# Kernel optimization log

Measured on AMD Instinct MI355X. Metric: run time of the kernel, lower is better.

Reference implementation:

```python
import jax, jax.numpy as jnp
import numpy as np

# dims
IMG = 24; B = 2; C = 3; N = IMG * IMG + 1        # 577 tokens (patch size 1 + cls)
DIM = 512; DEPTH = 2; H = 8; DH = 64; MLP = 2048; NCLS = 1000
SW = 32      # sliding window size
CB = 16      # compress block size
CS = 4       # compress block sliding stride
SB = 64      # selection block size
KSEL = 4     # num selected blocks


def _ln(x, g, b):
    m = x.mean(-1, keepdims=True)
    v = ((x - m) ** 2).mean(-1, keepdims=True)
    return (x - m) * jax.lax.rsqrt(v + 1e-5) * g + b


# gather rows per (batch, head): t [n, d], i [n, m] -> [n, m, d]
_gather = jax.vmap(jax.vmap(lambda t, i: t[i]))


def _sparse_attn(x, Wq, Wk, Wv, Wg, Wo, kpe, vpe, Wkc, Wvc):
    """Native-sparse-attention (non-causal): compress + top-k block select + sliding window,
    combined with per-head sigmoid gates computed from the input."""
    b, n, _ = x.shape
    split = lambda t: t.reshape(b, n, H, DH).transpose(0, 2, 1, 3)   # [b,h,n,dh]
    q = split(x @ Wq); k = split(x @ Wk); v = split(x @ Wv)
    scale = DH ** -0.5

    # ---- compressed branch: overlapping blocks of size CB, stride CS, MLP-compressed ----
    nc = -(-n // CS)
    pad = (nc - 1) * CS + CB - n
    kp = jnp.pad(k, ((0, 0), (0, 0), (0, pad), (0, 0)))
    vp = jnp.pad(v, ((0, 0), (0, 0), (0, pad), (0, 0)))
    widx = jnp.arange(nc)[:, None] * CS + jnp.arange(CB)[None, :]    # [nc, CB]
    kw = kp[:, :, widx] + kpe                                        # [b,h,nc,CB,dh]
    vw = vp[:, :, widx] + vpe
    ck = kw.reshape(b, H, nc, CB * DH) @ Wkc                         # [b,h,nc,dh]
    cv = vw.reshape(b, H, nc, CB * DH) @ Wvc
    sc = jnp.einsum('bhid,bhjd->bhij', q, ck) * scale                # [b,h,n,nc]
    pc = jax.nn.softmax(sc, axis=-1)
    out_c = jnp.einsum('bhij,bhjd->bhid', pc, cv)

    # ---- selection branch: map compressed-block scores to selection blocks, top-k ----
    ns = -(-n // SB)
    centers = jnp.clip((jnp.arange(nc) * CS + CB // 2) // SB, 0, ns - 1)
    M = jax.nn.one_hot(centers, ns, dtype=pc.dtype)                  # [nc, ns]
    imp = jnp.einsum('bhij,js->bhis', pc, M)                         # [b,h,n,ns]
    _, selb = jax.lax.top_k(imp, KSEL)                               # [b,h,n,KSEL]
    tok = (selb[..., None] * SB + jnp.arange(SB)).reshape(b, H, n, KSEL * SB)
    mask = tok < n
    tokc = jnp.minimum(tok, n - 1)
    kg = _gather(k, tokc)                                            # [b,h,n,KSEL*SB,dh]
    vg = _gather(v, tokc)
    ss = jnp.einsum('bhid,bhikd->bhik', q, kg) * scale
    ss = jnp.where(mask, ss, -jnp.inf)
    ps = jax.nn.softmax(ss, axis=-1)
    out_s = jnp.einsum('bhik,bhikd->bhid', ps, vg)

    # ---- sliding window branch ----
    off = jnp.arange(SW) - SW // 2
    pos = jnp.arange(n)[:, None] + off                               # [n, SW]
    wmask = (pos >= 0) & (pos < n)
    posc = jnp.clip(pos, 0, n - 1)
    kwn = k[:, :, posc]; vwn = v[:, :, posc]                         # [b,h,n,SW,dh]
    sw = jnp.einsum('bhid,bhiwd->bhiw', q, kwn) * scale
    sw = jnp.where(wmask, sw, -jnp.inf)
    pw = jax.nn.softmax(sw, axis=-1)
    out_w = jnp.einsum('bhiw,bhiwd->bhid', pw, vwn)

    # ---- gated combine ----
    g = jax.nn.sigmoid(x @ Wg).reshape(b, n, H, 3).transpose(0, 2, 1, 3)  # [b,h,n,3]
    out = g[..., 0:1] * out_c + g[..., 1:2] * out_s + g[..., 2:3] * out_w
    return out.transpose(0, 2, 1, 3).reshape(b, n, H * DH) @ Wo


def _forward(img, patch_w, patch_b, pos_emb, cls_tok, ln1_g, ln1_b, Wq, Wk, Wv,
             Wg, Wo, kpe, vpe, Wkc, Wvc, ln2_g, ln2_b, ff_w1, ff_b1, ff_w2,
             ff_b2, hln_g, hln_b, head_w, head_b):
    b = img.shape[0]
    # patch size 1: b c h w -> b (h w) c, then linear embed
    x = img.transpose(0, 2, 3, 1).reshape(b, IMG * IMG, C) @ patch_w + patch_b
    x = jnp.concatenate([jnp.broadcast_to(cls_tok, (b, 1, DIM)), x], axis=1)
    x = x + pos_emb[:, :x.shape[1]]
    for l in range(DEPTH):
        h = _ln(x, ln1_g[l], ln1_b[l])
        x = _sparse_attn(h, Wq[l], Wk[l], Wv[l], Wg[l], Wo[l], kpe[l], vpe[l], Wkc[l], Wvc[l]) + x
        h = _ln(x, ln2_g[l], ln2_b[l])
        x = (jax.nn.gelu(h @ ff_w1[l] + ff_b1[l]) @ ff_w2[l] + ff_b2[l]) + x
    x = _ln(x[:, 0], hln_g, hln_b)   # cls pool + head LayerNorm
    return x @ head_w + head_b


def setup_inputs() -> dict:
    key = jax.random.key(0)
    ks = jax.random.split(key, 20)
    rn = lambda k, shape, s=0.02: jax.random.normal(k, shape, dtype=jnp.float32) * s
    d = {}
    d['img'] = jax.random.normal(ks[0], (B, C, IMG, IMG), dtype=jnp.float32)
    d['patch_w'] = rn(ks[1], (C, DIM), 0.2)
    d['patch_b'] = jnp.zeros((DIM,), jnp.float32)
    d['pos_emb'] = rn(ks[2], (1, N, DIM))
    d['cls_tok'] = rn(ks[3], (1, 1, DIM))
    d['ln1_g'] = jnp.ones((DEPTH, DIM), jnp.float32)
    d['ln1_b'] = jnp.zeros((DEPTH, DIM), jnp.float32)
    d['Wq'] = rn(ks[4], (DEPTH, DIM, H * DH))
    d['Wk'] = rn(ks[5], (DEPTH, DIM, H * DH))
    d['Wv'] = rn(ks[6], (DEPTH, DIM, H * DH))
    d['Wg'] = rn(ks[7], (DEPTH, DIM, 3 * H))
    d['Wo'] = rn(ks[8], (DEPTH, H * DH, DIM))
    d['kpe'] = rn(ks[9], (DEPTH, CB, DH))
    d['vpe'] = rn(ks[10], (DEPTH, CB, DH))
    d['Wkc'] = rn(ks[11], (DEPTH, CB * DH, DH))
    d['Wvc'] = rn(ks[12], (DEPTH, CB * DH, DH))
    d['ln2_g'] = jnp.ones((DEPTH, DIM), jnp.float32)
    d['ln2_b'] = jnp.zeros((DEPTH, DIM), jnp.float32)
    d['ff_w1'] = rn(ks[13], (DEPTH, DIM, MLP))
    d['ff_b1'] = jnp.zeros((DEPTH, MLP), jnp.float32)
    d['ff_w2'] = rn(ks[14], (DEPTH, MLP, DIM))
    d['ff_b2'] = jnp.zeros((DEPTH, DIM), jnp.float32)
    d['hln_g'] = jnp.ones((DIM,), jnp.float32)
    d['hln_b'] = jnp.zeros((DIM,), jnp.float32)
    d['head_w'] = rn(ks[15], (DIM, NCLS))
    d['head_b'] = jnp.zeros((NCLS,), jnp.float32)
    return d


def reference(img, patch_w, patch_b, pos_emb, cls_tok, ln1_g, ln1_b, Wq, Wk, Wv,
              Wg, Wo, kpe, vpe, Wkc, Wvc, ln2_g, ln2_b, ff_w1, ff_b1, ff_w2,
              ff_b2, hln_g, hln_b, head_w, head_b):
    return _forward(img, patch_w, patch_b, pos_emb, cls_tok, ln1_g, ln1_b, Wq, Wk, Wv,
                    Wg, Wo, kpe, vpe, Wkc, Wvc, ln2_g, ln2_b, ff_w1, ff_b1, ff_w2,
                    ff_b2, hln_g, hln_b, head_w, head_b)
```

## Files before the change

kernel.cpp:

```cpp
#include <hip/hip_runtime.h>
#include <math.h>


#define NTOK 577
#define DIMD 512
#define NH 8
#define DHD 64
#define NC 145
#define NSB 10
#define KSELD 4
#define SBD 64
#define CBD 16
#define CSD 4
#define SWD 32
#define MLPD 2048
#define NCLSD 1000
#define BATCH 2
#define QKVN 1536
#define QKVNG 1600
#define SFSTRIDE 592
#define SCSTRIDE 160
#define PSTRIDE 832

typedef unsigned short ushort;
typedef __attribute__((ext_vector_type(8))) short short8;
typedef __attribute__((ext_vector_type(4))) short short4v;
typedef __attribute__((ext_vector_type(4))) float f32x4;

__device__ __forceinline__ ushort bf16_rne(float f) {
  union { float f; unsigned u; } v; v.f = f;
  unsigned u = v.u;
  unsigned r = (u + 0x7fffu + ((u >> 16) & 1u)) >> 16;
  return (ushort)r;
}
__device__ __forceinline__ float bf16_to_f(ushort s) {
  union { unsigned u; float f; } v; v.u = ((unsigned)s) << 16;
  return v.f;
}
__device__ __forceinline__ int imin(int a, int b) { return a < b ? a : b; }
__device__ __forceinline__ int imax(int a, int b) { return a > b ? a : b; }

__global__ void patch_kernel(const float* __restrict__ img, const float* __restrict__ pw,
                             const float* __restrict__ pb, const float* __restrict__ pos,
                             const float* __restrict__ cls, float* __restrict__ x) {
  int idx = blockIdx.x * 256 + threadIdx.x;
  const int total = BATCH * NTOK * DIMD;
  if (idx >= total) return;
  int d = idx & (DIMD - 1);
  int i = (idx / DIMD) % NTOK;
  int b = idx / (DIMD * NTOK);
  float val;
  if (i == 0) {
    val = cls[d];
  } else {
    int p = i - 1;
    val = pb[d];
#pragma unroll
    for (int c = 0; c < 3; ++c)
      val += img[b * 3 * 576 + c * 576 + p] * pw[c * DIMD + d];
  }
  x[idx] = val + pos[i * DIMD + d];
}

__global__ void ln_kernel(const float* __restrict__ x, const float* __restrict__ g,
                          const float* __restrict__ bb, ushort* __restrict__ out_bf,
                          float* __restrict__ out_f, long rstride) {
  int row = blockIdx.x;
  const float* xr = x + (long)row * rstride;
  int t = threadIdx.x;
  float a = xr[t], c = xr[t + 256];
  __shared__ float s1[256], s2[256];
  s1[t] = a + c;
  s2[t] = a * a + c * c;
  __syncthreads();
  for (int off = 128; off > 0; off >>= 1) {
    if (t < off) { s1[t] += s1[t + off]; s2[t] += s2[t + off]; }
    __syncthreads();
  }
  float m = s1[0] * (1.0f / 512.0f);
  float var = s2[0] * (1.0f / 512.0f) - m * m;
  float r = rsqrtf(var + 1e-5f);
  float o0 = (a - m) * r * g[t] + bb[t];
  float o1 = (c - m) * r * g[t + 256] + bb[t + 256];
  if (out_bf) {
    out_bf[(long)row * DIMD + t] = bf16_rne(o0);
    out_bf[(long)row * DIMD + t + 256] = bf16_rne(o1);
  }
  if (out_f) {
    out_f[(long)row * DIMD + t] = o0;
    out_f[(long)row * DIMD + t + 256] = o1;
  }
}

__global__ void wtrans_all_kernel(const float* __restrict__ Wq, const float* __restrict__ Wk,
                                  const float* __restrict__ Wv, const float* __restrict__ Wg,
                                  const float* __restrict__ Wo, const float* __restrict__ Wkc,
                                  const float* __restrict__ Wvc, const float* __restrict__ w1,
                                  const float* __restrict__ w2,
                                  ushort* __restrict__ wqkv_t, ushort* __restrict__ wo_t,
                                  ushort* __restrict__ w1_t, ushort* __restrict__ w2_t,
                                  ushort* __restrict__ wkc_t, ushort* __restrict__ wvc_t) {
  __shared__ float tile[32][33];
  int t = blockIdx.x;
  const float* W; ushort* Wt; int K, N, bx, by;
  if (t < 768) {
    int which = t >> 8, rr = t & 255;
    W = which == 0 ? Wq : (which == 1 ? Wk : Wv);
    Wt = wqkv_t + which * 512 * 512;
    K = 512; N = 512; bx = rr & 15; by = rr >> 4;
  } else if (t < 1024) {
    int rr = t - 768; W = Wo; Wt = wo_t; K = 512; N = 512; bx = rr & 15; by = rr >> 4;
  } else if (t < 2048) {
    int rr = t - 1024; W = w1; Wt = w1_t; K = 512; N = 2048; bx = rr & 63; by = rr >> 6;
  } else if (t < 3072) {
    int rr = t - 2048; W = w2; Wt = w2_t; K = 2048; N = 512; bx = rr & 15; by = rr >> 4;
  } else if (t < 3104) {
    int rr = t - 3072; W = Wg; Wt = wqkv_t + (long)1536 * 512; K = 512; N = 24; bx = rr & 1; by = rr >> 1;
  } else if (t < 3168) {
    int rr = t - 3104; W = Wkc; Wt = wkc_t; K = 1024; N = 64; bx = rr & 1; by = rr >> 1;
  } else {
    int rr = t - 3168; W = Wvc; Wt = wvc_t; K = 1024; N = 64; bx = rr & 1; by = rr >> 1;
  }
  int k0 = by * 32, n0 = bx * 32;
  int tx = threadIdx.x, ty = threadIdx.y;
#pragma unroll
  for (int r = 0; r < 32; r += 8)
    tile[ty + r][tx] = (n0 + tx < N) ? W[(long)(k0 + ty + r) * N + n0 + tx] : 0.f;
  __syncthreads();
#pragma unroll
  for (int r = 0; r < 32; r += 8)
    Wt[(long)(n0 + ty + r) * K + k0 + tx] = bf16_rne(tile[tx][ty + r]);
}

__global__ __launch_bounds__(256) void mfma_gemm(
    const ushort* __restrict__ A, const ushort* __restrict__ Bt,
    const float* __restrict__ bias,
    float* __restrict__ Cf, ushort* __restrict__ Cbf, float* __restrict__ gb,
    int M, int N, int K, int kSlice, int mode) {
  __shared__ short As[64][72];
  __shared__ short Bs[64][72];
  int tid = threadIdx.x;
  int lane = tid & 63, wave = tid >> 6;
  int wm = wave >> 1, wn = wave & 1;
  int rowBase = blockIdx.y * 64, colBase = blockIdx.x * 64;
  int m = lane & 15, kg = lane >> 4;
  int kBeg = blockIdx.z * kSlice;
  int kEnd = imin(K, kBeg + kSlice);
  f32x4 acc[2][2] = {};
  for (int k0 = kBeg; k0 < kEnd; k0 += 64) {
#pragma unroll
    for (int cc = 0; cc < 2; ++cc) {
      int c = tid * 2 + cc;
      int r = c >> 3, kc = c & 7;
      short8 av = {};
      int gr = rowBase + r;
      if (gr < M) av = *(const short8*)(A + (long)gr * K + k0 + kc * 8);
      *(short8*)&As[r][kc * 8] = av;
      short8 bv = *(const short8*)(Bt + (long)(colBase + r) * K + k0 + kc * 8);
      *(short8*)&Bs[r][kc * 8] = bv;
    }
    __syncthreads();
#pragma unroll
    for (int ks = 0; ks < 2; ++ks) {
      short8 a0 = *(const short8*)&As[wm * 32 + m][ks * 32 + kg * 8];
      short8 a1 = *(const short8*)&As[wm * 32 + 16 + m][ks * 32 + kg * 8];
      short8 b0 = *(const short8*)&Bs[wn * 32 + m][ks * 32 + kg * 8];
      short8 b1 = *(const short8*)&Bs[wn * 32 + 16 + m][ks * 32 + kg * 8];
      acc[0][0] = __builtin_amdgcn_mfma_f32_16x16x32_bf16(a0, b0, acc[0][0], 0, 0, 0);
      acc[0][1] = __builtin_amdgcn_mfma_f32_16x16x32_bf16(a0, b1, acc[0][1], 0, 0, 0);
      acc[1][0] = __builtin_amdgcn_mfma_f32_16x16x32_bf16(a1, b0, acc[1][0], 0, 0, 0);
      acc[1][1] = __builtin_amdgcn_mfma_f32_16x16x32_bf16(a1, b1, acc[1][1], 0, 0, 0);
    }
    __syncthreads();
  }
#pragma unroll
  for (int mt = 0; mt < 2; ++mt)
#pragma unroll
    for (int nt = 0; nt < 2; ++nt) {
      int col = colBase + wn * 32 + nt * 16 + m;
#pragma unroll
      for (int r = 0; r < 4; ++r) {
        int row = rowBase + wm * 32 + mt * 16 + kg * 4 + r;
        if (row >= M) continue;
        float v = acc[mt][nt][r];
        if (mode == 2) {
          if (col < QKVN) Cbf[(long)row * QKVN + col] = bf16_rne(v);
          else if (col < QKVNG) gb[(long)row * 64 + (col - QKVN)] = 1.f / (1.f + __expf(-v));
        } else if (mode == 1) {
          v += bias[col];
          float u = 0.7978845608028654f * (v + 0.044715f * v * v * v);
          v = 0.5f * v * (1.f + tanhf(u));
          Cbf[(long)row * N + col] = bf16_rne(v);
        } else {
          if (bias && blockIdx.z == 0) v += bias[col];
          atomicAdd(&Cf[(long)row * N + col], v);
        }
      }
    }
}

__global__ __launch_bounds__(256) void ckcv_gemm(
    const ushort* __restrict__ kwm, const ushort* __restrict__ vwm,
    const ushort* __restrict__ wkc_t, const ushort* __restrict__ wvc_t,
    ushort* __restrict__ ckb, ushort* __restrict__ cvb) {
  const ushort* A = blockIdx.z ? vwm : kwm;
  const ushort* Bt = blockIdx.z ? wvc_t : wkc_t;
  ushort* C = blockIdx.z ? cvb : ckb;
  const int M = BATCH * NH * NC, N = 64, K = 1024;
  __shared__ short As[64][72];
  __shared__ short Bs[64][72];
  int tid = threadIdx.x;
  int lane = tid & 63, wave = tid >> 6;
  int wm = wave >> 1, wn = wave & 1;
  int rowBase = blockIdx.y * 64;
  int m = lane & 15, kg = lane >> 4;
  f32x4 acc[2][2] = {};
  for (int k0 = 0; k0 < K; k0 += 64) {
#pragma unroll
    for (int cc = 0; cc < 2; ++cc) {
      int c = tid * 2 + cc;
      int r = c >> 3, kc = c & 7;
      short8 av = {};
      int gr = rowBase + r;
      if (gr < M) av = *(const short8*)(A + (long)gr * K + k0 + kc * 8);
      *(short8*)&As[r][kc * 8] = av;
      short8 bv = *(const short8*)(Bt + (long)r * K + k0 + kc * 8);
      *(short8*)&Bs[r][kc * 8] = bv;
    }
    __syncthreads();
#pragma unroll
    for (int ks = 0; ks < 2; ++ks) {
      short8 a0 = *(const short8*)&As[wm * 32 + m][ks * 32 + kg * 8];
      short8 a1 = *(const short8*)&As[wm * 32 + 16 + m][ks * 32 + kg * 8];
      short8 b0 = *(const short8*)&Bs[wn * 32 + m][ks * 32 + kg * 8];
      short8 b1 = *(const short8*)&Bs[wn * 32 + 16 + m][ks * 32 + kg * 8];
      acc[0][0] = __builtin_amdgcn_mfma_f32_16x16x32_bf16(a0, b0, acc[0][0], 0, 0, 0);
      acc[0][1] = __builtin_amdgcn_mfma_f32_16x16x32_bf16(a0, b1, acc[0][1], 0, 0, 0);
      acc[1][0] = __builtin_amdgcn_mfma_f32_16x16x32_bf16(a1, b0, acc[1][0], 0, 0, 0);
      acc[1][1] = __builtin_amdgcn_mfma_f32_16x16x32_bf16(a1, b1, acc[1][1], 0, 0, 0);
    }
    __syncthreads();
  }
#pragma unroll
  for (int mt = 0; mt < 2; ++mt)
#pragma unroll
    for (int nt = 0; nt < 2; ++nt) {
      int col = wn * 32 + nt * 16 + m;
#pragma unroll
      for (int r = 0; r < 4; ++r) {
        int row = rowBase + wm * 32 + mt * 16 + kg * 4 + r;
        if (row < M) C[(long)row * N + col] = bf16_rne(acc[mt][nt][r]);
      }
    }
}

__global__ __launch_bounds__(256) void score_kernel(
    const ushort* __restrict__ qkv_bf, const ushort* __restrict__ ckb,
    ushort* __restrict__ Sf, ushort* __restrict__ Scb, float scale) {
  __shared__ short As[64][72];
  __shared__ short Bs[64][72];
  int z = blockIdx.z;
  int b = z >> 3, h = z & 7;
  int i0 = blockIdx.y * 64;
  int xb = blockIdx.x;
  bool isC = xb >= 10;
  int j0 = (isC ? (xb - 10) : xb) * 64;
  int tid = threadIdx.x;
  int lane = tid & 63, wave = tid >> 6;
  int wm = wave >> 1, wn = wave & 1;
  const ushort* aBase = qkv_bf + (long)b * NTOK * QKVN + h * 64;
  const ushort* bBase = aBase + 512;
  const ushort* cBase = ckb + (long)z * NC * DHD;
#pragma unroll
  for (int rep = 0; rep < 4; ++rep) {
    int row = rep * 16 + (tid >> 4);
    int c4 = tid & 15;
    int gi = i0 + row;
    short4v a16 = {};
    if (gi < NTOK) a16 = *(const short4v*)(aBase + (long)gi * QKVN + c4 * 4);
    *(short4v*)&As[row][c4 * 4] = a16;
    int gj = j0 + row;
    short4v b16 = {};
    if (isC) {
      if (gj < NC) b16 = *(const short4v*)(cBase + (long)gj * DHD + c4 * 4);
    } else {
      if (gj < NTOK) b16 = *(const short4v*)(bBase + (long)gj * QKVN + c4 * 4);
    }
    *(short4v*)&Bs[row][c4 * 4] = b16;
  }
  __syncthreads();
  int m = lane & 15, kg = lane >> 4;
  f32x4 acc[2][2] = {};
#pragma unroll
  for (int ks = 0; ks < 2; ++ks) {
    short8 a0 = *(const short8*)&As[wm * 32 + m][ks * 32 + kg * 8];
    short8 a1 = *(const short8*)&As[wm * 32 + 16 + m][ks * 32 + kg * 8];
    short8 b0 = *(const short8*)&Bs[wn * 32 + m][ks * 32 + kg * 8];
    short8 b1 = *(const short8*)&Bs[wn * 32 + 16 + m][ks * 32 + kg * 8];
    acc[0][0] = __builtin_amdgcn_mfma_f32_16x16x32_bf16(a0, b0, acc[0][0], 0, 0, 0);
    acc[0][1] = __builtin_amdgcn_mfma_f32_16x16x32_bf16(a0, b1, acc[0][1], 0, 0, 0);
    acc[1][0] = __builtin_amdgcn_mfma_f32_16x16x32_bf16(a1, b0, acc[1][0], 0, 0, 0);
    acc[1][1] = __builtin_amdgcn_mfma_f32_16x16x32_bf16(a1, b1, acc[1][1], 0, 0, 0);
  }
  int nvalid = isC ? NC : NTOK;
  int sstride = isC ? SCSTRIDE : SFSTRIDE;
  ushort* Sz = (isC ? Scb : Sf) + (long)z * NTOK * sstride;
#pragma unroll
  for (int mt = 0; mt < 2; ++mt)
#pragma unroll
    for (int nt = 0; nt < 2; ++nt) {
      int col = j0 + wn * 32 + nt * 16 + m;
#pragma unroll
      for (int r = 0; r < 4; ++r) {
        int row = i0 + wm * 32 + mt * 16 + kg * 4 + r;
        if (row < NTOK && col < nvalid)
          Sz[(long)row * sstride + col] = bf16_rne(acc[mt][nt][r] * scale);
      }
    }
}

__global__ void kwbuild_kernel(const ushort* __restrict__ qkv_bf,
                               const float* __restrict__ kpe, const float* __restrict__ vpe,
                               ushort* __restrict__ kwm, ushort* __restrict__ vwm) {
  int r = blockIdx.x;
  int j = r % NC;
  int bh = r / NC;
  int h = bh & 7, b = bh >> 3;
  int t = threadIdx.x >> 4;
  int d4 = threadIdx.x & 15;
  int tok = j * CSD + t;
  float k0 = 0.f, k1 = 0.f, k2 = 0.f, k3 = 0.f, v0 = 0.f, v1 = 0.f, v2 = 0.f, v3 = 0.f;
  if (tok < NTOK) {
    const ushort* base = qkv_bf + (long)(b * NTOK + tok) * QKVN + h * DHD + d4 * 4;
    short4v kv = *(const short4v*)(base + 512);
    short4v vv = *(const short4v*)(base + 1024);
    k0 = bf16_to_f((ushort)kv.x); k1 = bf16_to_f((ushort)kv.y);
    k2 = bf16_to_f((ushort)kv.z); k3 = bf16_to_f((ushort)kv.w);
    v0 = bf16_to_f((ushort)vv.x); v1 = bf16_to_f((ushort)vv.y);
    v2 = bf16_to_f((ushort)vv.z); v3 = bf16_to_f((ushort)vv.w);
  }
  float4 kp = *(const float4*)(kpe + t * DHD + d4 * 4);
  float4 vp = *(const float4*)(vpe + t * DHD + d4 * 4);
  short4v ko, vo;
  ko.x = (short)bf16_rne(k0 + kp.x); ko.y = (short)bf16_rne(k1 + kp.y);
  ko.z = (short)bf16_rne(k2 + kp.z); ko.w = (short)bf16_rne(k3 + kp.w);
  vo.x = (short)bf16_rne(v0 + vp.x); vo.y = (short)bf16_rne(v1 + vp.y);
  vo.z = (short)bf16_rne(v2 + vp.z); vo.w = (short)bf16_rne(v3 + vp.w);
  long ob = (long)r * 1024 + t * DHD + d4 * 4;
  *(short4v*)(kwm + ob) = ko;
  *(short4v*)(vwm + ob) = vo;
}

__global__ void vtrans_kernel(const ushort* __restrict__ qkv_bf, const ushort* __restrict__ cvb,
                              ushort* __restrict__ Vt) {
  int kt = blockIdx.x;
  int z = blockIdx.y;
  int b = z >> 3, h = z & 7;
  __shared__ short tile[64][72];
  int tid = threadIdx.x;
  int r = tid >> 2, seg = tid & 3;
  short8 a0 = {}, a1 = {};
  if (kt < 10) {
    int tok = kt * 64 + r;
    if (tok < NTOK) {
      const ushort* src = qkv_bf + (long)(b * NTOK + tok) * QKVN + 1024 + h * 64 + seg * 16;
      a0 = *(const short8*)src;
      a1 = *(const short8*)(src + 8);
    }
  } else {
    int cr = (kt - 10) * 64 + r;
    if (cr < NC) {
      const ushort* src = cvb + ((long)z * NC + cr) * DHD + seg * 16;
      a0 = *(const short8*)src;
      a1 = *(const short8*)(src + 8);
    }
  }
  *(short8*)&tile[r][seg * 16] = a0;
  *(short8*)&tile[r][seg * 16 + 8] = a1;
  __syncthreads();
  int d = tid >> 2;
  short8 o0, o1;
#pragma unroll
  for (int q = 0; q < 8; ++q) o0[q] = tile[seg * 16 + q][d];
#pragma unroll
  for (int q = 0; q < 8; ++q) o1[q] = tile[seg * 16 + 8 + q][d];
  ushort* dst = Vt + ((long)z * 64 + d) * PSTRIDE + kt * 64 + seg * 16;
  *(short8*)dst = o0;
  *(short8*)(dst + 8) = o1;
}

__global__ __launch_bounds__(256, 4) void prob_kernel(
    const ushort* __restrict__ Sf, const ushort* __restrict__ Scb,
    const float* __restrict__ gb, ushort* __restrict__ P) {
  int qt = blockIdx.x % NC;
  int z = blockIdx.x / NC;
  int h = z & 7, b = z >> 3;
  int tid = threadIdx.x, lane = tid & 63, w = tid >> 6;
  int i0 = qt * 4 + w;
  bool valid = i0 < NTOK;
  int i = imin(i0, NTOK - 1);

  __shared__ float scL[4][192];
  __shared__ float ssL[4][256];
  __shared__ float swL[4][32];
  __shared__ float impL[4][16];
  __shared__ int selL[4][KSELD];
  float* sc = scL[w]; float* ss = ssL[w];
  float* swv = swL[w]; float* imp = impL[w]; int* sel = selL[w];

  const ushort* scRow = Scb + ((long)z * NTOK + i) * SCSTRIDE;
  const ushort* sfRow = Sf + ((long)z * NTOK + i) * SFSTRIDE;

  float e[3], mC = -1e30f;
#pragma unroll
  for (int c = 0; c < 3; ++c) {
    int j = c * 64 + lane;
    float s = bf16_to_f(scRow[imin(j, NC - 1)]);
    s = (j < NC) ? s : -1e30f;
    e[c] = s;
    mC = fmaxf(mC, s);
  }
#pragma unroll
  for (int msk = 1; msk < 64; msk <<= 1) mC = fmaxf(mC, __shfl_xor(mC, msk, 64));
  float sumC = 0.f;
#pragma unroll
  for (int c = 0; c < 3; ++c) {
    float ev = (e[c] > -1e29f) ? __expf(e[c] - mC) : 0.f;
    sc[c * 64 + lane] = ev;
    sumC += ev;
  }
#pragma unroll
  for (int msk = 1; msk < 64; msk <<= 1) sumC += __shfl_xor(sumC, msk, 64);
  __syncthreads();

  if (lane < NSB) {
    int lo = imax(0, 16 * lane - 2), hi = imin(NC - 1, 16 * lane + 13);
    float s = 0.f;
    for (int j = lo; j <= hi; ++j) s += sc[j];
    imp[lane] = s;
  }
  __syncthreads();
  if (lane == 0) {
    unsigned used = 0;
    for (int r = 0; r < KSELD; ++r) {
      int bi = 0; float bv = -1e30f;
      for (int s = 0; s < NSB; ++s)
        if (!((used >> s) & 1u) && imp[s] > bv) { bv = imp[s]; bi = s; }
      used |= 1u << bi;
      sel[r] = bi;
    }
  }
  __syncthreads();

  float es[4], mS = -1e30f;
#pragma unroll
  for (int c = 0; c < 4; ++c) {
    int tok = sel[c] * SBD + lane;
    float s = bf16_to_f(sfRow[imin(tok, NTOK - 1)]);
    s = (tok < NTOK) ? s : -1e30f;
    es[c] = s;
    mS = fmaxf(mS, s);
  }
#pragma unroll
  for (int msk = 1; msk < 64; msk <<= 1) mS = fmaxf(mS, __shfl_xor(mS, msk, 64));
  float sumS = 0.f;
#pragma unroll
  for (int c = 0; c < 4; ++c) {
    float ev = (es[c] > -1e29f) ? __expf(es[c] - mS) : 0.f;
    ss[c * 64 + lane] = ev;
    sumS += ev;
  }
#pragma unroll
  for (int msk = 1; msk < 64; msk <<= 1) sumS += __shfl_xor(sumS, msk, 64);

  float sw_s;
  {
    int pos = i + (lane & 31) - SWD / 2;
    float s = bf16_to_f(sfRow[imin(imax(pos, 0), NTOK - 1)]);
    sw_s = (pos >= 0 && pos < NTOK) ? s : -1e30f;
  }
  float mW = sw_s;
#pragma unroll
  for (int msk = 1; msk < 32; msk <<= 1) mW = fmaxf(mW, __shfl_xor(mW, msk, 64));
  float ew = (sw_s > -1e29f) ? __expf(sw_s - mW) : 0.f;
  float sumW = ew;
#pragma unroll
  for (int msk = 1; msk < 32; msk <<= 1) sumW += __shfl_xor(sumW, msk, 64);
  if (lane < SWD) swv[lane] = ew;
  __syncthreads();

  if (!valid) return;
  const float* gp = gb + (long)(b * NTOK + i) * 64 + h * 3;
  float rC = gp[0] / sumC, rS = gp[1] / sumS, rW = gp[2] / sumW;
  ushort* prow = P + ((long)z * NTOK + i0) * PSTRIDE;
#pragma unroll
  for (int c = 0; c < 10; ++c) {
    int col = c * 64 + lane;
    float val = 0.f;
#pragma unroll
    for (int r = 0; r < 4; ++r)
      if (sel[r] == c) val += rS * ss[r * 64 + lane];
    int t = col - i + 16;
    if (t >= 0 && t < SWD && col < NTOK) val += rW * swv[t];
    prow[col] = bf16_rne(val);
  }
#pragma unroll
  for (int c = 0; c < 3; ++c) {
    int j = c * 64 + lane;
    float val = (j < NC) ? rC * sc[j] : 0.f;
    prow[640 + j] = bf16_rne(val);
  }
}

__global__ __launch_bounds__(256) void pv_gemm(const ushort* __restrict__ P,
                                               const ushort* __restrict__ Vt,
                                               ushort* __restrict__ comb) {
  __shared__ short As[64][72];
  __shared__ short Bs[64][72];
  int z = blockIdx.y;
  int b = z >> 3, h = z & 7;
  int rowBase = blockIdx.x * 64;
  int tid = threadIdx.x;
  int lane = tid & 63, wave = tid >> 6;
  int wm = wave >> 1, wn = wave & 1;
  const ushort* Pz = P + (long)z * NTOK * PSTRIDE;
  const ushort* Vz = Vt + (long)z * 64 * PSTRIDE;
  int m = lane & 15, kg = lane >> 4;
  f32x4 acc[2][2] = {};
  for (int k0 = 0; k0 < PSTRIDE; k0 += 64) {
#pragma unroll
    for (int cc = 0; cc < 2; ++cc) {
      int c = tid * 2 + cc;
      int r = c >> 3, kc = c & 7;
      short8 av = {};
      int gr = rowBase + r;
      if (gr < NTOK) av = *(const short8*)(Pz + (long)gr * PSTRIDE + k0 + kc * 8);
      *(short8*)&As[r][kc * 8] = av;
      short8 bv = *(const short8*)(Vz + (long)r * PSTRIDE + k0 + kc * 8);
      *(short8*)&Bs[r][kc * 8] = bv;
    }
    __syncthreads();
#pragma unroll
    for (int ks = 0; ks < 2; ++ks) {
      short8 a0 = *(const short8*)&As[wm * 32 + m][ks * 32 + kg * 8];
      short8 a1 = *(const short8*)&As[wm * 32 + 16 + m][ks * 32 + kg * 8];
      short8 b0 = *(const short8*)&Bs[wn * 32 + m][ks * 32 + kg * 8];
      short8 b1 = *(const short8*)&Bs[wn * 32 + 16 + m][ks * 32 + kg * 8];
      acc[0][0] = __builtin_amdgcn_mfma_f32_16x16x32_bf16(a0, b0, acc[0][0], 0, 0, 0);
      acc[0][1] = __builtin_amdgcn_mfma_f32_16x16x32_bf16(a0, b1, acc[0][1], 0, 0, 0);
      acc[1][0] = __builtin_amdgcn_mfma_f32_16x16x32_bf16(a1, b0, acc[1][0], 0, 0, 0);
      acc[1][1] = __builtin_amdgcn_mfma_f32_16x16x32_bf16(a1, b1, acc[1][1], 0, 0, 0);
    }
    __syncthreads();
  }
#pragma unroll
  for (int mt = 0; mt < 2; ++mt)
#pragma unroll
    for (int nt = 0; nt < 2; ++nt) {
      int col = wn * 32 + nt * 16 + m;
#pragma unroll
      for (int r = 0; r < 4; ++r) {
        int row = rowBase + wm * 32 + mt * 16 + kg * 4 + r;
        if (row < NTOK)
          comb[(long)(b * NTOK + row) * DIMD + h * 64 + col] = bf16_rne(acc[mt][nt][r]);
      }
    }
}

__global__ void head_kernel(const float* __restrict__ hfin, const float* __restrict__ W,
                            const float* __restrict__ bias, float* __restrict__ out) {
  __shared__ float hs[512];
  int bidx = blockIdx.y;
  int t = threadIdx.x;
  hs[t] = hfin[bidx * 512 + t];
  hs[t + 256] = hfin[bidx * 512 + t + 256];
  __syncthreads();
  int col = blockIdx.x * 256 + t;
  if (col < NCLSD) {
    float acc = bias[col];
#pragma unroll 8
    for (int k = 0; k < 512; ++k) acc += hs[k] * W[(long)k * NCLSD + col];
    out[bidx * NCLSD + col] = acc;
  }
}

extern "C" void kernel_launch(void* const* d_in, const int* in_sizes, int n_in,
                              void* d_out, int out_size, void* d_ws, size_t ws_size,
                              hipStream_t stream) {
  const float* img     = (const float*)d_in[0];
  const float* patch_w = (const float*)d_in[1];
  const float* patch_b = (const float*)d_in[2];
  const float* pos_emb = (const float*)d_in[3];
  const float* cls_tok = (const float*)d_in[4];
  const float* ln1_g   = (const float*)d_in[5];
  const float* ln1_b   = (const float*)d_in[6];
  const float* Wq      = (const float*)d_in[7];
  const float* Wk      = (const float*)d_in[8];
  const float* Wv      = (const float*)d_in[9];
  const float* Wg      = (const float*)d_in[10];
  const float* Wo      = (const float*)d_in[11];
  const float* kpe     = (const float*)d_in[12];
  const float* vpe     = (const float*)d_in[13];
  const float* Wkc     = (const float*)d_in[14];
  const float* Wvc     = (const float*)d_in[15];
  const float* ln2_g   = (const float*)d_in[16];
  const float* ln2_b   = (const float*)d_in[17];
  const float* ff_w1   = (const float*)d_in[18];
  const float* ff_b1   = (const float*)d_in[19];
  const float* ff_w2   = (const float*)d_in[20];
  const float* ff_b2   = (const float*)d_in[21];
  const float* hln_g   = (const float*)d_in[22];
  const float* hln_b   = (const float*)d_in[23];
  const float* head_w  = (const float*)d_in[24];
  const float* head_b  = (const float*)d_in[25];
  float* out = (float*)d_out;

  char* p = (char*)d_ws;
  const long MROW = (long)BATCH * NTOK;
  float* x       = (float*)p;  p += MROW * DIMD * 4;
  ushort* qkv_bf = (ushort*)p; p += MROW * QKVN * 2;
  ushort* h_bf   = (ushort*)p; p += MROW * DIMD * 2;
  ushort* comb_bf= (ushort*)p; p += MROW * DIMD * 2;
  float* gb      = (float*)p;  p += MROW * 64 * 4;
  ushort* ckb    = (ushort*)p; p += (long)BATCH * NH * NC * DHD * 2;
  ushort* cvb    = (ushort*)p; p += (long)BATCH * NH * NC * DHD * 2;
  ushort* Vt     = (ushort*)p; p += (long)BATCH * NH * 64 * PSTRIDE * 2;
  ushort* Scb    = (ushort*)p; p += (long)BATCH * NH * NTOK * SCSTRIDE * 2;
  float* hfin    = (float*)p;  p += BATCH * DIMD * 4;
  ushort* wqkv_t = (ushort*)p; p += (long)1664 * DIMD * 2;
  ushort* wo_t   = (ushort*)p; p += (long)DIMD * DIMD * 2;
  ushort* w1_t   = (ushort*)p; p += (long)MLPD * DIMD * 2;
  ushort* w2_t   = (ushort*)p; p += (long)DIMD * MLPD * 2;
  ushort* wkc_t  = (ushort*)p; p += (long)64 * 1024 * 2;
  ushort* wvc_t  = (ushort*)p; p += (long)64 * 1024 * 2;
  ushort* kwm    = (ushort*)p;
  ushort* vwm    = kwm + (long)BATCH * NH * NC * 1024;
  ushort* P      = kwm;
  p += (long)BATCH * NH * NTOK * PSTRIDE * 2;
  ushort* Sf     = (ushort*)p;
  ushort* ff1_bf = Sf;
  p += (long)BATCH * NH * NTOK * SFSTRIDE * 2;

  const int M = (int)MROW;
  const int MB64 = (M + 63) / 64;
  const int MCK = BATCH * NH * NC;
  const float scale = 0.125f;
  dim3 thrT(32, 8);

  patch_kernel<<<(M * DIMD + 255) / 256, 256, 0, stream>>>(img, patch_w, patch_b, pos_emb, cls_tok, x);

  for (int l = 0; l < 2; ++l) {
    const float* Wq_l  = Wq + (long)l * DIMD * DIMD;
    const float* Wk_l  = Wk + (long)l * DIMD * DIMD;
    const float* Wv_l  = Wv + (long)l * DIMD * DIMD;
    const float* Wg_l  = Wg + (long)l * DIMD * 3 * NH;
    const float* Wo_l  = Wo + (long)l * DIMD * DIMD;
    const float* kpe_l = kpe + (long)l * CBD * DHD;
    const float* vpe_l = vpe + (long)l * CBD * DHD;
    const float* Wkc_l = Wkc + (long)l * CBD * DHD * DHD;
    const float* Wvc_l = Wvc + (long)l * CBD * DHD * DHD;
    const float* w1_l  = ff_w1 + (long)l * DIMD * MLPD;
    const float* b1_l  = ff_b1 + (long)l * MLPD;
    const float* w2_l  = ff_w2 + (long)l * MLPD * DIMD;
    const float* b2_l  = ff_b2 + (long)l * DIMD;

    wtrans_all_kernel<<<3232, thrT, 0, stream>>>(Wq_l, Wk_l, Wv_l, Wg_l, Wo_l, Wkc_l, Wvc_l,
                                                 w1_l, w2_l, wqkv_t, wo_t, w1_t, w2_t,
                                                 wkc_t, wvc_t);
    ln_kernel<<<M, 256, 0, stream>>>(x, ln1_g + (long)l * DIMD, ln1_b + (long)l * DIMD, h_bf, nullptr, DIMD);
    mfma_gemm<<<dim3(QKVNG / 64, MB64), 256, 0, stream>>>(h_bf, wqkv_t, nullptr, nullptr, qkv_bf, gb, M, QKVNG, DIMD, DIMD, 2);
    kwbuild_kernel<<<MCK, 256, 0, stream>>>(qkv_bf, kpe_l, vpe_l, kwm, vwm);
    ckcv_gemm<<<dim3(1, (MCK + 63) / 64, 2), 256, 0, stream>>>(kwm, vwm, wkc_t, wvc_t, ckb, cvb);
    vtrans_kernel<<<dim3(13, BATCH * NH), 256, 0, stream>>>(qkv_bf, cvb, Vt);
    score_kernel<<<dim3(13, 10, BATCH * NH), 256, 0, stream>>>(qkv_bf, ckb, Sf, Scb, scale);
    prob_kernel<<<BATCH * NH * NC, 256, 0, stream>>>(Sf, Scb, gb, P);
    pv_gemm<<<dim3(10, BATCH * NH), 256, 0, stream>>>(P, Vt, comb_bf);
    mfma_gemm<<<dim3(DIMD / 64, MB64, 2), 256, 0, stream>>>(comb_bf, wo_t, nullptr, x, nullptr, nullptr, M, DIMD, DIMD, 256, 4);
    ln_kernel<<<M, 256, 0, stream>>>(x, ln2_g + (long)l * DIMD, ln2_b + (long)l * DIMD, h_bf, nullptr, DIMD);
    mfma_gemm<<<dim3(MLPD / 64, MB64), 256, 0, stream>>>(h_bf, w1_t, b1_l, nullptr, ff1_bf, nullptr, M, MLPD, DIMD, DIMD, 1);
    mfma_gemm<<<dim3(DIMD / 64, MB64, 4), 256, 0, stream>>>(ff1_bf, w2_t, b2_l, x, nullptr, nullptr, M, DIMD, MLPD, 512, 4);
  }

  ln_kernel<<<BATCH, 256, 0, stream>>>(x, hln_g, hln_b, nullptr, hfin, (long)NTOK * DIMD);
  head_kernel<<<dim3((NCLSD + 255) / 256, BATCH), 256, 0, stream>>>(hfin, head_w, head_b, out);
}
```

Before: 388.4 us.

## Batch weight transposes, fuse kw-build with V transpose, write cv into Vt, fuse head LN

Converts the weights for both layers in one launch instead of once per layer. Merges the window-build and V-transpose kernels into a single launch. The compressed-V GEMM now runs transposed and writes straight into the Vt buffer, which removes the cvb intermediate and its copy. The final layernorm is folded into the head kernel, whose dot product is split across four K-slices per column for more parallelism. Together these cut launch count and intermediate traffic, at the cost of a larger weight buffer and uncoalesced transposed stores of cv into Vt.

```diff
diff --git a/kernel.cpp b/kernel.cpp
--- a/kernel.cpp
+++ b/kernel.cpp
@@ -21,6 +21,7 @@
 #define SFSTRIDE 592
 #define SCSTRIDE 160
 #define PSTRIDE 832
+#define MCKD 2320
 
 typedef unsigned short ushort;
 typedef __attribute__((ext_vector_type(8))) short short8;
@@ -63,10 +64,9 @@
 }
 
 __global__ void ln_kernel(const float* __restrict__ x, const float* __restrict__ g,
-                          const float* __restrict__ bb, ushort* __restrict__ out_bf,
-                          float* __restrict__ out_f, long rstride) {
+                          const float* __restrict__ bb, ushort* __restrict__ out_bf) {
   int row = blockIdx.x;
-  const float* xr = x + (long)row * rstride;
+  const float* xr = x + (long)row * DIMD;
   int t = threadIdx.x;
   float a = xr[t], c = xr[t + 256];
   __shared__ float s1[256], s2[256];
@@ -80,16 +80,8 @@
   float m = s1[0] * (1.0f / 512.0f);
   float var = s2[0] * (1.0f / 512.0f) - m * m;
   float r = rsqrtf(var + 1e-5f);
-  float o0 = (a - m) * r * g[t] + bb[t];
-  float o1 = (c - m) * r * g[t + 256] + bb[t + 256];
-  if (out_bf) {
-    out_bf[(long)row * DIMD + t] = bf16_rne(o0);
-    out_bf[(long)row * DIMD + t + 256] = bf16_rne(o1);
-  }
-  if (out_f) {
-    out_f[(long)row * DIMD + t] = o0;
-    out_f[(long)row * DIMD + t + 256] = o1;
-  }
+  out_bf[(long)row * DIMD + t] = bf16_rne((a - m) * r * g[t] + bb[t]);
+  out_bf[(long)row * DIMD + t + 256] = bf16_rne((c - m) * r * g[t + 256] + bb[t + 256]);
 }
 
 __global__ void wtrans_all_kernel(const float* __restrict__ Wq, const float* __restrict__ Wk,
@@ -101,25 +93,33 @@
                                   ushort* __restrict__ w1_t, ushort* __restrict__ w2_t,
                                   ushort* __restrict__ wkc_t, ushort* __restrict__ wvc_t) {
   __shared__ float tile[32][33];
+  int l = blockIdx.y;
   int t = blockIdx.x;
   const float* W; ushort* Wt; int K, N, bx, by;
   if (t < 768) {
     int which = t >> 8, rr = t & 255;
-    W = which == 0 ? Wq : (which == 1 ? Wk : Wv);
-    Wt = wqkv_t + which * 512 * 512;
+    W = (which == 0 ? Wq : (which == 1 ? Wk : Wv)) + (long)l * 512 * 512;
+    Wt = wqkv_t + (long)l * QKVNG * 512 + which * 512 * 512;
     K = 512; N = 512; bx = rr & 15; by = rr >> 4;
   } else if (t < 1024) {
-    int rr = t - 768; W = Wo; Wt = wo_t; K = 512; N = 512; bx = rr & 15; by = rr >> 4;
+    int rr = t - 768; W = Wo + (long)l * 512 * 512; Wt = wo_t + (long)l * 512 * 512;
+    K = 512; N = 512; bx = rr & 15; by = rr >> 4;
   } else if (t < 2048) {
-    int rr = t - 1024; W = w1; Wt = w1_t; K = 512; N = 2048; bx = rr & 63; by = rr >> 6;
+    int rr = t - 1024; W = w1 + (long)l * 512 * 2048; Wt = w1_t + (long)l * 2048 * 512;
+    K = 512; N = 2048; bx = rr & 63; by = rr >> 6;
   } else if (t < 3072) {
-    int rr = t - 2048; W = w2; Wt = w2_t; K = 2048; N = 512; bx = rr & 15; by = rr >> 4;
+    int rr = t - 2048; W = w2 + (long)l * 2048 * 512; Wt = w2_t + (long)l * 512 * 2048;
+    K = 2048; N = 512; bx = rr & 15; by = rr >> 4;
   } else if (t < 3104) {
-    int rr = t - 3072; W = Wg; Wt = wqkv_t + (long)1536 * 512; K = 512; N = 24; bx = rr & 1; by = rr >> 1;
+    int rr = t - 3072; W = Wg + (long)l * 512 * 24;
+    Wt = wqkv_t + (long)l * QKVNG * 512 + (long)1536 * 512;
+    K = 512; N = 24; bx = rr & 1; by = rr >> 1;
   } else if (t < 3168) {
-    int rr = t - 3104; W = Wkc; Wt = wkc_t; K = 1024; N = 64; bx = rr & 1; by = rr >> 1;
+    int rr = t - 3104; W = Wkc + (long)l * 1024 * 64; Wt = wkc_t + (long)l * 64 * 1024;
+    K = 1024; N = 64; bx = rr & 1; by = rr >> 1;
   } else {
-    int rr = t - 3168; W = Wvc; Wt = wvc_t; K = 1024; N = 64; bx = rr & 1; by = rr >> 1;
+    int rr = t - 3168; W = Wvc + (long)l * 1024 * 64; Wt = wvc_t + (long)l * 64 * 1024;
+    K = 1024; N = 64; bx = rr & 1; by = rr >> 1;
   }
   int k0 = by * 32, n0 = bx * 32;
   int tx = threadIdx.x, ty = threadIdx.y;
@@ -202,17 +202,20 @@
 __global__ __launch_bounds__(256) void ckcv_gemm(
     const ushort* __restrict__ kwm, const ushort* __restrict__ vwm,
     const ushort* __restrict__ wkc_t, const ushort* __restrict__ wvc_t,
-    ushort* __restrict__ ckb, ushort* __restrict__ cvb) {
-  const ushort* A = blockIdx.z ? vwm : kwm;
-  const ushort* Bt = blockIdx.z ? wvc_t : wkc_t;
-  ushort* C = blockIdx.z ? cvb : ckb;
-  const int M = BATCH * NH * NC, N = 64, K = 1024;
+    ushort* __restrict__ ckb, ushort* __restrict__ Vt) {
+  const int K = 1024;
+  bool cvpath = blockIdx.z != 0;
+  const ushort* A  = cvpath ? wvc_t : kwm;
+  const ushort* Bt = cvpath ? vwm : wkc_t;
+  int rowBase = cvpath ? 0 : blockIdx.y * 64;
+  int colBase = cvpath ? blockIdx.y * 64 : 0;
+  int aRows = cvpath ? 64 : MCKD;
+  int bRows = cvpath ? MCKD : 64;
   __shared__ short As[64][72];
   __shared__ short Bs[64][72];
   int tid = threadIdx.x;
   int lane = tid & 63, wave = tid >> 6;
   int wm = wave >> 1, wn = wave & 1;
-  int rowBase = blockIdx.y * 64;
   int m = lane & 15, kg = lane >> 4;
   f32x4 acc[2][2] = {};
   for (int k0 = 0; k0 < K; k0 += 64) {
@@ -221,10 +224,10 @@
       int c = tid * 2 + cc;
       int r = c >> 3, kc = c & 7;
       short8 av = {};
-      int gr = rowBase + r;
-      if (gr < M) av = *(const short8*)(A + (long)gr * K + k0 + kc * 8);
+      if (rowBase + r < aRows) av = *(const short8*)(A + (long)(rowBase + r) * K + k0 + kc * 8);
       *(short8*)&As[r][kc * 8] = av;
-      short8 bv = *(const short8*)(Bt + (long)r * K + k0 + kc * 8);
+      short8 bv = {};
+      if (colBase + r < bRows) bv = *(const short8*)(Bt + (long)(colBase + r) * K + k0 + kc * 8);
       *(short8*)&Bs[r][kc * 8] = bv;
     }
     __syncthreads();
@@ -245,11 +248,19 @@
   for (int mt = 0; mt < 2; ++mt)
 #pragma unroll
     for (int nt = 0; nt < 2; ++nt) {
-      int col = wn * 32 + nt * 16 + m;
+      int col = colBase + wn * 32 + nt * 16 + m;
 #pragma unroll
       for (int r = 0; r < 4; ++r) {
         int row = rowBase + wm * 32 + mt * 16 + kg * 4 + r;
-        if (row < M) C[(long)row * N + col] = bf16_rne(acc[mt][nt][r]);
+        float v = acc[mt][nt][r];
+        if (!cvpath) {
+          if (row < MCKD) ckb[(long)row * DHD + col] = bf16_rne(v);
+        } else {
+          if (col < MCKD) {
+            int z16 = col / NC, j = col - z16 * NC;
+            Vt[((long)z16 * 64 + row) * PSTRIDE + 640 + j] = bf16_rne(v);
+          }
+        }
       }
     }
 }
@@ -319,74 +330,65 @@
     }
 }
 
-__global__ void kwbuild_kernel(const ushort* __restrict__ qkv_bf,
-                               const float* __restrict__ kpe, const float* __restrict__ vpe,
-                               ushort* __restrict__ kwm, ushort* __restrict__ vwm) {
-  int r = blockIdx.x;
-  int j = r % NC;
-  int bh = r / NC;
-  int h = bh & 7, b = bh >> 3;
-  int t = threadIdx.x >> 4;
-  int d4 = threadIdx.x & 15;
-  int tok = j * CSD + t;
-  float k0 = 0.f, k1 = 0.f, k2 = 0.f, k3 = 0.f, v0 = 0.f, v1 = 0.f, v2 = 0.f, v3 = 0.f;
-  if (tok < NTOK) {
-    const ushort* base = qkv_bf + (long)(b * NTOK + tok) * QKVN + h * DHD + d4 * 4;
-    short4v kv = *(const short4v*)(base + 512);
-    short4v vv = *(const short4v*)(base + 1024);
-    k0 = bf16_to_f((ushort)kv.x); k1 = bf16_to_f((ushort)kv.y);
-    k2 = bf16_to_f((ushort)kv.z); k3 = bf16_to_f((ushort)kv.w);
-    v0 = bf16_to_f((ushort)vv.x); v1 = bf16_to_f((ushort)vv.y);
-    v2 = bf16_to_f((ushort)vv.z); v3 = bf16_to_f((ushort)vv.w);
-  }
-  float4 kp = *(const float4*)(kpe + t * DHD + d4 * 4);
-  float4 vp = *(const float4*)(vpe + t * DHD + d4 * 4);
-  short4v ko, vo;
-  ko.x = (short)bf16_rne(k0 + kp.x); ko.y = (short)bf16_rne(k1 + kp.y);
-  ko.z = (short)bf16_rne(k2 + kp.z); ko.w = (short)bf16_rne(k3 + kp.w);
-  vo.x = (short)bf16_rne(v0 + vp.x); vo.y = (short)bf16_rne(v1 + vp.y);
-  vo.z = (short)bf16_rne(v2 + vp.z); vo.w = (short)bf16_rne(v3 + vp.w);
-  long ob = (long)r * 1024 + t * DHD + d4 * 4;
-  *(short4v*)(kwm + ob) = ko;
-  *(short4v*)(vwm + ob) = vo;
-}
-
-__global__ void vtrans_kernel(const ushort* __restrict__ qkv_bf, const ushort* __restrict__ cvb,
-                              ushort* __restrict__ Vt) {
-  int kt = blockIdx.x;
-  int z = blockIdx.y;
-  int b = z >> 3, h = z & 7;
+__global__ void kwvt_kernel(const ushort* __restrict__ qkv_bf,
+                            const float* __restrict__ kpe, const float* __restrict__ vpe,
+                            ushort* __restrict__ kwm, ushort* __restrict__ vwm,
+                            ushort* __restrict__ Vt) {
   __shared__ short tile[64][72];
-  int tid = threadIdx.x;
-  int r = tid >> 2, seg = tid & 3;
-  short8 a0 = {}, a1 = {};
-  if (kt < 10) {
+  int bid = blockIdx.x;
+  if (bid < MCKD) {
+    int j = bid % NC;
+    int bh = bid / NC;
+    int h = bh & 7, b = bh >> 3;
+    int t = threadIdx.x >> 4;
+    int d4 = threadIdx.x & 15;
+    int tok = j * CSD + t;
+    float k0 = 0.f, k1 = 0.f, k2 = 0.f, k3 = 0.f, v0 = 0.f, v1 = 0.f, v2 = 0.f, v3 = 0.f;
+    if (tok < NTOK) {
+      const ushort* base = qkv_bf + (long)(b * NTOK + tok) * QKVN + h * DHD + d4 * 4;
+      short4v kv = *(const short4v*)(base + 512);
+      short4v vv = *(const short4v*)(base + 1024);
+      k0 = bf16_to_f((ushort)kv.x); k1 = bf16_to_f((ushort)kv.y);
+      k2 = bf16_to_f((ushort)kv.z); k3 = bf16_to_f((ushort)kv.w);
+      v0 = bf16_to_f((ushort)vv.x); v1 = bf16_to_f((ushort)vv.y);
+      v2 = bf16_to_f((ushort)vv.z); v3 = bf16_to_f((ushort)vv.w);
+    }
+    float4 kp = *(const float4*)(kpe + t * DHD + d4 * 4);
+    float4 vp = *(const float4*)(vpe + t * DHD + d4 * 4);
+    short4v ko, vo;
+    ko.x = (short)bf16_rne(k0 + kp.x); ko.y = (short)bf16_rne(k1 + kp.y);
+    ko.z = (short)bf16_rne(k2 + kp.z); ko.w = (short)bf16_rne(k3 + kp.w);
+    vo.x = (short)bf16_rne(v0 + vp.x); vo.y = (short)bf16_rne(v1 + vp.y);
+    vo.z = (short)bf16_rne(v2 + vp.z); vo.w = (short)bf16_rne(v3 + vp.w);
+    long ob = (long)bid * 1024 + t * DHD + d4 * 4;
+    *(short4v*)(kwm + ob) = ko;
+    *(short4v*)(vwm + ob) = vo;
+  } else {
+    int t = bid - MCKD;
+    int kt = t % 10, z = t / 10;
+    int b = z >> 3, h = z & 7;
+    int tid = threadIdx.x;
+    int r = tid >> 2, seg = tid & 3;
+    short8 a0 = {}, a1 = {};
     int tok = kt * 64 + r;
     if (tok < NTOK) {
       const ushort* src = qkv_bf + (long)(b * NTOK + tok) * QKVN + 1024 + h * 64 + seg * 16;
       a0 = *(const short8*)src;
       a1 = *(const short8*)(src + 8);
     }
-  } else {
-    int cr = (kt - 10) * 64 + r;
-    if (cr < NC) {
-      const ushort* src = cvb + ((long)z * NC + cr) * DHD + seg * 16;
-      a0 = *(const short8*)src;
-      a1 = *(const short8*)(src + 8);
-    }
-  }
-  *(short8*)&tile[r][seg * 16] = a0;
-  *(short8*)&tile[r][seg * 16 + 8] = a1;
-  __syncthreads();
-  int d = tid >> 2;
-  short8 o0, o1;
-#pragma unroll
-  for (int q = 0; q < 8; ++q) o0[q] = tile[seg * 16 + q][d];
-#pragma unroll
-  for (int q = 0; q < 8; ++q) o1[q] = tile[seg * 16 + 8 + q][d];
-  ushort* dst = Vt + ((long)z * 64 + d) * PSTRIDE + kt * 64 + seg * 16;
-  *(short8*)dst = o0;
-  *(short8*)(dst + 8) = o1;
+    *(short8*)&tile[r][seg * 16] = a0;
+    *(short8*)&tile[r][seg * 16 + 8] = a1;
+    __syncthreads();
+    int d = tid >> 2;
+    short8 o0, o1;
+#pragma unroll
+    for (int q = 0; q < 8; ++q) o0[q] = tile[seg * 16 + q][d];
+#pragma unroll
+    for (int q = 0; q < 8; ++q) o1[q] = tile[seg * 16 + 8 + q][d];
+    ushort* dst = Vt + ((long)z * 64 + d) * PSTRIDE + kt * 64 + seg * 16;
+    *(short8*)dst = o0;
+    *(short8*)(dst + 8) = o1;
+  }
 }
 
 __global__ __launch_bounds__(256, 4) void prob_kernel(
@@ -567,20 +569,42 @@
     }
 }
 
-__global__ void head_kernel(const float* __restrict__ hfin, const float* __restrict__ W,
+__global__ void head_kernel(const float* __restrict__ x, const float* __restrict__ hg,
+                            const float* __restrict__ hb, const float* __restrict__ W,
                             const float* __restrict__ bias, float* __restrict__ out) {
+  int b = blockIdx.y;
+  int tid = threadIdx.x;
+  const float* xr = x + (long)b * NTOK * DIMD;
+  __shared__ float red1[256], red2[256];
+  float a = xr[tid], c = xr[tid + 256];
+  red1[tid] = a + c;
+  red2[tid] = a * a + c * c;
+  __syncthreads();
+  for (int off = 128; off > 0; off >>= 1) {
+    if (tid < off) { red1[tid] += red1[tid + off]; red2[tid] += red2[tid + off]; }
+    __syncthreads();
+  }
+  float m = red1[0] * (1.f / 512.f);
+  float var = red2[0] * (1.f / 512.f) - m * m;
+  float rs = rsqrtf(var + 1e-5f);
   __shared__ float hs[512];
-  int bidx = blockIdx.y;
-  int t = threadIdx.x;
-  hs[t] = hfin[bidx * 512 + t];
-  hs[t + 256] = hfin[bidx * 512 + t + 256];
-  __syncthreads();
-  int col = blockIdx.x * 256 + t;
+  hs[tid] = (a - m) * rs * hg[tid] + hb[tid];
+  hs[tid + 256] = (c - m) * rs * hg[tid + 256] + hb[tid + 256];
+  __syncthreads();
+  int col = blockIdx.x * 64 + (tid & 63);
+  int ks = tid >> 6;
+  float acc = 0.f;
   if (col < NCLSD) {
-    float acc = bias[col];
-#pragma unroll 8
-    for (int k = 0; k < 512; ++k) acc += hs[k] * W[(long)k * NCLSD + col];
-    out[bidx * NCLSD + col] = acc;
+    for (int k = ks * 128; k < ks * 128 + 128; ++k)
+      acc += hs[k] * W[(long)k * NCLSD + col];
+  }
+  __shared__ float part[4][64];
+  part[ks][tid & 63] = acc;
+  __syncthreads();
+  if (tid < 64) {
+    int c2 = blockIdx.x * 64 + tid;
+    if (c2 < NCLSD)
+      out[b * NCLSD + c2] = part[0][tid] + part[1][tid] + part[2][tid] + part[3][tid] + bias[c2];
   }
 }
 
@@ -622,19 +646,17 @@
   ushort* h_bf   = (ushort*)p; p += MROW * DIMD * 2;
   ushort* comb_bf= (ushort*)p; p += MROW * DIMD * 2;
   float* gb      = (float*)p;  p += MROW * 64 * 4;
-  ushort* ckb    = (ushort*)p; p += (long)BATCH * NH * NC * DHD * 2;
-  ushort* cvb    = (ushort*)p; p += (long)BATCH * NH * NC * DHD * 2;
+  ushort* ckb    = (ushort*)p; p += (long)MCKD * DHD * 2;
   ushort* Vt     = (ushort*)p; p += (long)BATCH * NH * 64 * PSTRIDE * 2;
   ushort* Scb    = (ushort*)p; p += (long)BATCH * NH * NTOK * SCSTRIDE * 2;
-  float* hfin    = (float*)p;  p += BATCH * DIMD * 4;
-  ushort* wqkv_t = (ushort*)p; p += (long)1664 * DIMD * 2;
-  ushort* wo_t   = (ushort*)p; p += (long)DIMD * DIMD * 2;
-  ushort* w1_t   = (ushort*)p; p += (long)MLPD * DIMD * 2;
-  ushort* w2_t   = (ushort*)p; p += (long)DIMD * MLPD * 2;
-  ushort* wkc_t  = (ushort*)p; p += (long)64 * 1024 * 2;
-  ushort* wvc_t  = (ushort*)p; p += (long)64 * 1024 * 2;
+  ushort* wqkv_t = (ushort*)p; p += 2L * QKVNG * DIMD * 2;
+  ushort* wo_t   = (ushort*)p; p += 2L * DIMD * DIMD * 2;
+  ushort* w1_t   = (ushort*)p; p += 2L * MLPD * DIMD * 2;
+  ushort* w2_t   = (ushort*)p; p += 2L * DIMD * MLPD * 2;
+  ushort* wkc_t  = (ushort*)p; p += 2L * 64 * 1024 * 2;
+  ushort* wvc_t  = (ushort*)p; p += 2L * 64 * 1024 * 2;
   ushort* kwm    = (ushort*)p;
-  ushort* vwm    = kwm + (long)BATCH * NH * NC * 1024;
+  ushort* vwm    = kwm + (long)MCKD * 1024;
   ushort* P      = kwm;
   p += (long)BATCH * NH * NTOK * PSTRIDE * 2;
   ushort* Sf     = (ushort*)p;
@@ -643,44 +665,38 @@
 
   const int M = (int)MROW;
   const int MB64 = (M + 63) / 64;
-  const int MCK = BATCH * NH * NC;
   const float scale = 0.125f;
   dim3 thrT(32, 8);
 
   patch_kernel<<<(M * DIMD + 255) / 256, 256, 0, stream>>>(img, patch_w, patch_b, pos_emb, cls_tok, x);
+  wtrans_all_kernel<<<dim3(3232, 2), thrT, 0, stream>>>(Wq, Wk, Wv, Wg, Wo, Wkc, Wvc,
+                                                        ff_w1, ff_w2, wqkv_t, wo_t, w1_t, w2_t,
+                                                        wkc_t, wvc_t);
 
   for (int l = 0; l < 2; ++l) {
-    const float* Wq_l  = Wq + (long)l * DIMD * DIMD;
-    const float* Wk_l  = Wk + (long)l * DIMD * DIMD;
-    const float* Wv_l  = Wv + (long)l * DIMD * DIMD;
-    const float* Wg_l  = Wg + (long)l * DIMD * 3 * NH;
-    const float* Wo_l  = Wo + (long)l * DIMD * DIMD;
+    const ushort* wqkv_l = wqkv_t + (long)l * QKVNG * DIMD;
+    const ushort* wo_l   = wo_t + (long)l * DIMD * DIMD;
+    const ushort* w1t_l  = w1_t + (long)l * MLPD * DIMD;
+    const ushort* w2t_l  = w2_t + (long)l * DIMD * MLPD;
+    const ushort* wkc_l  = wkc_t + (long)l * 64 * 1024;
+    const ushort* wvc_l  = wvc_t + (long)l * 64 * 1024;
     const float* kpe_l = kpe + (long)l * CBD * DHD;
     const float* vpe_l = vpe + (long)l * CBD * DHD;
-    const float* Wkc_l = Wkc + (long)l * CBD * DHD * DHD;
-    const float* Wvc_l = Wvc + (long)l * CBD * DHD * DHD;
-    const float* w1_l  = ff_w1 + (long)l * DIMD * MLPD;
     const float* b1_l  = ff_b1 + (long)l * MLPD;
-    const float* w2_l  = ff_w2 + (long)l * MLPD * DIMD;
     const float* b2_l  = ff_b2 + (long)l * DIMD;
 
-    wtrans_all_kernel<<<3232, thrT, 0, stream>>>(Wq_l, Wk_l, Wv_l, Wg_l, Wo_l, Wkc_l, Wvc_l,
-                                                 w1_l, w2_l, wqkv_t, wo_t, w1_t, w2_t,
-                                                 wkc_t, wvc_t);
-    ln_kernel<<<M, 256, 0, stream>>>(x, ln1_g + (long)l * DIMD, ln1_b + (long)l * DIMD, h_bf, nullptr, DIMD);
-    mfma_gemm<<<dim3(QKVNG / 64, MB64), 256, 0, stream>>>(h_bf, wqkv_t, nullptr, nullptr, qkv_bf, gb, M, QKVNG, DIMD, DIMD, 2);
-    kwbuild_kernel<<<MCK, 256, 0, stream>>>(qkv_bf, kpe_l, vpe_l, kwm, vwm);
-    ckcv_gemm<<<dim3(1, (MCK + 63) / 64, 2), 256, 0, stream>>>(kwm, vwm, wkc_t, wvc_t, ckb, cvb);
-    vtrans_kernel<<<dim3(13, BATCH * NH), 256, 0, stream>>>(qkv_bf, cvb, Vt);
+    ln_kernel<<<M, 256, 0, stream>>>(x, ln1_g + (long)l * DIMD, ln1_b + (long)l * DIMD, h_bf);
+    mfma_gemm<<<dim3(QKVNG / 64, MB64), 256, 0, stream>>>(h_bf, wqkv_l, nullptr, nullptr, qkv_bf, gb, M, QKVNG, DIMD, DIMD, 2);
+    kwvt_kernel<<<MCKD + 160, 256, 0, stream>>>(qkv_bf, kpe_l, vpe_l, kwm, vwm, Vt);
+    ckcv_gemm<<<dim3(1, (MCKD + 63) / 64, 2), 256, 0, stream>>>(kwm, vwm, wkc_l, wvc_l, ckb, Vt);
     score_kernel<<<dim3(13, 10, BATCH * NH), 256, 0, stream>>>(qkv_bf, ckb, Sf, Scb, scale);
     prob_kernel<<<BATCH * NH * NC, 256, 0, stream>>>(Sf, Scb, gb, P);
     pv_gemm<<<dim3(10, BATCH * NH), 256, 0, stream>>>(P, Vt, comb_bf);
-    mfma_gemm<<<dim3(DIMD / 64, MB64, 2), 256, 0, stream>>>(comb_bf, wo_t, nullptr, x, nullptr, nullptr, M, DIMD, DIMD, 256, 4);
-    ln_kernel<<<M, 256, 0, stream>>>(x, ln2_g + (long)l * DIMD, ln2_b + (long)l * DIMD, h_bf, nullptr, DIMD);
-    mfma_gemm<<<dim3(MLPD / 64, MB64), 256, 0, stream>>>(h_bf, w1_t, b1_l, nullptr, ff1_bf, nullptr, M, MLPD, DIMD, DIMD, 1);
-    mfma_gemm<<<dim3(DIMD / 64, MB64, 4), 256, 0, stream>>>(ff1_bf, w2_t, b2_l, x, nullptr, nullptr, M, DIMD, MLPD, 512, 4);
-  }
-
-  ln_kernel<<<BATCH, 256, 0, stream>>>(x, hln_g, hln_b, nullptr, hfin, (long)NTOK * DIMD);
-  head_kernel<<<dim3((NCLSD + 255) / 256, BATCH), 256, 0, stream>>>(hfin, head_w, head_b, out);
-}
+    mfma_gemm<<<dim3(DIMD / 64, MB64, 2), 256, 0, stream>>>(comb_bf, wo_l, nullptr, x, nullptr, nullptr, M, DIMD, DIMD, 256, 4);
+    ln_kernel<<<M, 256, 0, stream>>>(x, ln2_g + (long)l * DIMD, ln2_b + (long)l * DIMD, h_bf);
+    mfma_gemm<<<dim3(MLPD / 64, MB64), 256, 0, stream>>>(h_bf, w1t_l, b1_l, nullptr, ff1_bf, nullptr, M, MLPD, DIMD, DIMD, 1);
+    mfma_gemm<<<dim3(DIMD / 64, MB64, 4), 256, 0, stream>>>(ff1_bf, w2t_l, b2_l, x, nullptr, nullptr, M, DIMD, MLPD, 512, 4);
+  }
+
+  head_kernel<<<dim3(16, BATCH), 256, 0, stream>>>(x, hln_g, hln_b, head_w, head_b, out);
+}
```

Measured after the change: 379.4 us. -2.3%, faster.
